# Optimization experiments

Hardware: AMD Instinct MI355X
Metric: run time of the kernel (lower is better)

Reference implementation:

```python
import jax, jax.numpy as jnp
import numpy as np

N_NODES = 50000
N_EDGES = 800000
N_PAIRS = 200000
IN_DIM = 128
HID = 64
OUT_DIM = 1


def _gat_layer(x, W, a_l, a_r, src, dst, n_nodes):
    # Single-head GAT (DGL-style): z = xW; attention logits from learned
    # left/right vectors; softmax over incoming edges of each dst node.
    z = x @ W                                   # [N, H]
    el = z @ a_l                                # [N]
    er = z @ a_r                                # [N]
    e = jax.nn.leaky_relu(el[src] + er[dst], 0.2)   # [E]
    emax = jax.ops.segment_max(e, dst, num_segments=n_nodes)  # [N]
    ex = jnp.exp(e - emax[dst])                 # [E], stable softmax numerator
    denom = jax.ops.segment_sum(ex, dst, num_segments=n_nodes)  # [N]
    msg = ex[:, None] * z[src]                  # [E, H]
    agg = jax.ops.segment_sum(msg, dst, num_segments=n_nodes)   # [N, H]
    return agg / jnp.maximum(denom, 1e-9)[:, None]


def setup_inputs() -> dict:
    key = jax.random.key(0)
    ks = jax.random.split(key, 10)
    feat = jax.random.normal(ks[0], (N_NODES, IN_DIM), dtype=jnp.float32)
    src = jax.random.randint(ks[1], (N_EDGES,), 0, N_NODES, dtype=jnp.int32)
    dst = jax.random.randint(ks[2], (N_EDGES,), 0, N_NODES, dtype=jnp.int32)
    # query pairs: take existing edges so the has_edges_between mask is true
    pair_src = src[:N_PAIRS]
    pair_dst = dst[:N_PAIRS]
    s1 = 1.0 / np.sqrt(IN_DIM)
    s2 = 1.0 / np.sqrt(HID)
    W1 = jax.random.normal(ks[3], (IN_DIM, HID), dtype=jnp.float32) * s1
    al1 = jax.random.normal(ks[4], (HID,), dtype=jnp.float32) * s2
    ar1 = jax.random.normal(ks[5], (HID,), dtype=jnp.float32) * s2
    W2 = jax.random.normal(ks[6], (HID, HID), dtype=jnp.float32) * s2
    al2 = jax.random.normal(ks[7], (HID,), dtype=jnp.float32) * s2
    ar2 = jax.random.normal(ks[8], (HID,), dtype=jnp.float32) * s2
    Wc = jax.random.normal(ks[9], (2 * HID, OUT_DIM), dtype=jnp.float32) * s2
    bc = jnp.zeros((OUT_DIM,), dtype=jnp.float32)
    return {"feat": feat, "W1": W1, "al1": al1, "ar1": ar1,
            "W2": W2, "al2": al2, "ar2": ar2, "Wc": Wc, "bc": bc,
            "src": src, "dst": dst, "pair_src": pair_src, "pair_dst": pair_dst}


def reference(feat, W1, al1, ar1, W2, al2, ar2, Wc, bc, src, dst, pair_src, pair_dst):
    src = src.astype(jnp.int32)
    dst = dst.astype(jnp.int32)
    # two hetero GAT layers (single ntype -> mean aggregate is identity) + ReLU
    h = jax.nn.relu(_gat_layer(feat, W1, al1, ar1, src, dst, N_NODES))
    h = jax.nn.relu(_gat_layer(h, W2, al2, ar2, src, dst, N_NODES))
    # has_edges_between(pair_src, pair_dst): membership test via sorted edge keys
    ekeys = src.astype(jnp.int64) * N_NODES + dst.astype(jnp.int64)
    skeys = jnp.sort(ekeys)
    pkeys = pair_src.astype(jnp.int64) * N_NODES + pair_dst.astype(jnp.int64)
    idx = jnp.clip(jnp.searchsorted(skeys, pkeys), 0, N_EDGES - 1)
    mask = (skeys[idx] == pkeys)                 # [P] bool
    # gather endpoint embeddings, concat, classify, sigmoid; invalid rows -> 0
    hs = h[pair_src]                             # [P, H]
    hd = h[pair_dst]                             # [P, H]
    h_pair = jnp.concatenate([hs, hd], axis=1)   # [P, 2H]
    out = jax.nn.sigmoid(h_pair @ Wc + bc)       # [P, OUT]
    return out * mask[:, None].astype(out.dtype)
```

## Files before the change

kernel.cpp:

```cpp
#include <hip/hip_runtime.h>
#include <cstdint>

#define N_NODES 50000
#define N_EDGES 800000
#define N_PAIRS 200000
#define IN_DIM 128
#define HID 64
#define N_WAVES_GEMM (N_NODES / 16)
#define NBIN 196
#define NCH 320
#define CHUNK ((N_EDGES + NCH - 1) / NCH)
#define MHIST (NBIN * NCH)
#define SBG ((MHIST + 255) / 256)
#define MB_GEMM ((N_WAVES_GEMM + 3) / 4)
#define NODE_BLOCKS ((N_NODES + 3) / 4)
#define MEMBER_BLOCKS (N_PAIRS / 32)
#define SEG_T 1024

typedef __attribute__((ext_vector_type(8))) short bf16x8;
typedef __attribute__((ext_vector_type(4))) float f32x4;

__device__ __forceinline__ unsigned short bf16_rne(float f) {
    unsigned u = __float_as_uint(f);
    unsigned t = u + 0x7FFFu + ((u >> 16) & 1u);
    return (unsigned short)(t >> 16);
}
__device__ __forceinline__ void bf2f(unsigned u, float& a, float& b) {
    a = __uint_as_float(u << 16);
    b = __uint_as_float(u & 0xFFFF0000u);
}

__global__ __launch_bounds__(256) void hist_prep(
    const int* __restrict__ dst, int* __restrict__ histHi,
    const float* __restrict__ W1, const float* __restrict__ W2,
    unsigned short* __restrict__ w1hi, unsigned short* __restrict__ w1lo,
    unsigned short* __restrict__ w2hi, unsigned short* __restrict__ w2lo)
{
    const int t = threadIdx.x, b = blockIdx.x;
    if (b < NCH) {
        __shared__ int hist[256];
        hist[t] = 0; __syncthreads();
        const int beg = b * CHUNK, end = min(beg + CHUNK, N_EDGES);
        for (int e = beg + t; e < end; e += 256) atomicAdd(&hist[dst[e] >> 8], 1);
        __syncthreads();
        if (t < NBIN) histHi[t * NCH + b] = hist[t];
    } else {
        int tid = (b - NCH) * 256 + t;
        if (tid < 8192) {
            int jj = tid & 7, lane = (tid >> 3) & 63, tt = (tid >> 9) & 3, ks = tid >> 11;
            int k = ks * 32 + (lane >> 4) * 8 + jj;
            int n = tt * 16 + (lane & 15);
            float f = W1[k * HID + n];
            unsigned short hi = bf16_rne(f);
            float fhi = __uint_as_float(((unsigned)hi) << 16);
            w1hi[tid] = hi;
            w1lo[tid] = bf16_rne(f - fhi);
        }
        if (tid < 4096) {
            int jj = tid & 7, lane = (tid >> 3) & 63, tt = (tid >> 9) & 3, ks = tid >> 11;
            int k = ks * 32 + (lane >> 4) * 8 + jj;
            int n = tt * 16 + (lane & 15);
            float f = W2[k * HID + n];
            unsigned short hi = bf16_rne(f);
            float fhi = __uint_as_float(((unsigned)hi) << 16);
            w2hi[tid] = hi;
            w2lo[tid] = bf16_rne(f - fhi);
        }
    }
}

__global__ __launch_bounds__(256) void scan1g(
    int* __restrict__ histHi, int* __restrict__ bsums)
{
    __shared__ int sh[256];
    const int t = threadIdx.x;
    const int i = blockIdx.x * 256 + t;
    int v = (i < MHIST) ? histHi[i] : 0;
    sh[t] = v; __syncthreads();
    #pragma unroll
    for (int off = 1; off < 256; off <<= 1) {
        int x = sh[t];
        int a = (t >= off) ? sh[t - off] : 0;
        __syncthreads();
        sh[t] = x + a;
        __syncthreads();
    }
    if (i < MHIST) histHi[i] = sh[t] - v;
    if (t == 255) bsums[blockIdx.x] = sh[255];
}

__device__ __forceinline__ void scan_bsums(const int* __restrict__ bsums,
                                           int* sh, int* exb, int t)
{
    int v = (t < SBG) ? bsums[t] : 0;
    sh[t] = v; __syncthreads();
    #pragma unroll
    for (int off = 1; off < 256; off <<= 1) {
        int x = sh[t];
        int a = (t >= off) ? sh[t - off] : 0;
        __syncthreads();
        sh[t] = x + a;
        __syncthreads();
    }
    exb[t] = sh[t] - v;
    __syncthreads();
}

__device__ __forceinline__ void gemm1_body(
    int wave, int lane,
    const float* __restrict__ x,
    const unsigned short* __restrict__ whi, const unsigned short* __restrict__ wlo,
    const float* __restrict__ al, const float* __restrict__ ar,
    unsigned short* __restrict__ z, float* __restrict__ el, float* __restrict__ er)
{
    const int i0 = wave * 16;
    const int m = lane & 15, quad = lane >> 4;
    f32x4 acc[4] = {{0.f,0.f,0.f,0.f},{0.f,0.f,0.f,0.f},{0.f,0.f,0.f,0.f},{0.f,0.f,0.f,0.f}};
    const float* xrow = x + (size_t)(i0 + m) * IN_DIM;

    #pragma unroll 1
    for (int ks = 0; ks < 4; ++ks) {
        const float4 xv0 = *(const float4*)&xrow[ks * 32 + quad * 8];
        const float4 xv1 = *(const float4*)&xrow[ks * 32 + quad * 8 + 4];
        float xs[8] = {xv0.x, xv0.y, xv0.z, xv0.w, xv1.x, xv1.y, xv1.z, xv1.w};
        bf16x8 ahi, alo;
        #pragma unroll
        for (int jj = 0; jj < 8; ++jj) {
            unsigned short hb = bf16_rne(xs[jj]);
            float fhi = __uint_as_float(((unsigned)hb) << 16);
            ahi[jj] = (short)hb;
            alo[jj] = (short)bf16_rne(xs[jj] - fhi);
        }
        #pragma unroll
        for (int t = 0; t < 4; ++t) {
            const bf16x8 bhi = *(const bf16x8*)&whi[(((ks * 4 + t) * 64) + lane) * 8];
            const bf16x8 blo = *(const bf16x8*)&wlo[(((ks * 4 + t) * 64) + lane) * 8];
            acc[t] = __builtin_amdgcn_mfma_f32_16x16x32_bf16(ahi, bhi, acc[t], 0, 0, 0);
            acc[t] = __builtin_amdgcn_mfma_f32_16x16x32_bf16(ahi, blo, acc[t], 0, 0, 0);
            acc[t] = __builtin_amdgcn_mfma_f32_16x16x32_bf16(alo, bhi, acc[t], 0, 0, 0);
        }
    }
    #pragma unroll
    for (int r = 0; r < 4; ++r) {
        const int row = quad * 4 + r;
        float se = 0.f, sr = 0.f;
        #pragma unroll
        for (int t = 0; t < 4; ++t) {
            float v = acc[t][r];
            z[(size_t)(i0 + row) * HID + t * 16 + m] = bf16_rne(v);
            se = fmaf(v, al[t * 16 + m], se);
            sr = fmaf(v, ar[t * 16 + m], sr);
        }
        #pragma unroll
        for (int off = 1; off < 16; off <<= 1) {
            se += __shfl_xor(se, off, 64);
            sr += __shfl_xor(sr, off, 64);
        }
        if (m == 0) { el[i0 + row] = se; er[i0 + row] = sr; }
    }
}

__global__ __launch_bounds__(256) void scatter_gemm1(
    const int* __restrict__ src, const int* __restrict__ dst,
    const int* __restrict__ histEx, const int* __restrict__ bsums,
    unsigned* __restrict__ pairs,
    const float* __restrict__ x,
    const unsigned short* __restrict__ whi, const unsigned short* __restrict__ wlo,
    const float* __restrict__ al, const float* __restrict__ ar,
    unsigned short* __restrict__ z, float* __restrict__ el, float* __restrict__ er)
{
    const int b = blockIdx.x;
    if (b < NCH) {
        __shared__ int sh[256], exb[256], base[256];
        const int t = threadIdx.y * 64 + threadIdx.x;
        scan_bsums(bsums, sh, exb, t);
        if (t < NBIN) {
            int idx = t * NCH + b;
            base[t] = histEx[idx] + exb[idx >> 8];
        }
        __syncthreads();
        const int beg = b * CHUNK, end = min(beg + CHUNK, N_EDGES);
        for (int e = beg + t; e < end; e += 256) {
            int s = src[e], d = dst[e];
            int pos = atomicAdd(&base[d >> 8], 1);
            pairs[pos] = ((unsigned)s << 16) | (unsigned)d;
        }
    } else {
        const int wave = (b - NCH) * 4 + threadIdx.y;
        if (wave < N_WAVES_GEMM)
            gemm1_body(wave, threadIdx.x, x, whi, wlo, al, ar, z, el, er);
    }
}

__global__ __launch_bounds__(SEG_T) void seg_sort(
    const unsigned* __restrict__ pairs, const int* __restrict__ histEx,
    const int* __restrict__ bsums,
    int* __restrict__ row_start, unsigned short* __restrict__ csr_src)
{
    __shared__ int sh[256], exb[256], hist[256], sc[256], offs[256];
    const int t = threadIdx.x, b = blockIdx.x;

    {
        int v = 0;
        if (t < 256) { v = (t < SBG) ? bsums[t] : 0; sh[t] = v; }
        __syncthreads();
        #pragma unroll
        for (int off = 1; off < 256; off <<= 1) {
            int x = 0, a = 0;
            if (t < 256) { x = sh[t]; a = (t >= off) ? sh[t - off] : 0; }
            __syncthreads();
            if (t < 256) sh[t] = x + a;
            __syncthreads();
        }
        if (t < 256) exb[t] = sh[t] - v;
        __syncthreads();
    }

    const int i0 = b * NCH;
    const int segStart = histEx[i0] + exb[i0 >> 8];
    int segEnd = N_EDGES;
    if (b < NBIN - 1) {
        const int i1 = (b + 1) * NCH;
        segEnd = histEx[i1] + exb[i1 >> 8];
    }

    if (t < 256) hist[t] = 0;
    __syncthreads();
    for (int i = segStart + t; i < segEnd; i += SEG_T)
        atomicAdd(&hist[pairs[i] & 255], 1);
    __syncthreads();

    int v = 0;
    if (t < 256) { v = hist[t]; sc[t] = v; }
    __syncthreads();
    #pragma unroll
    for (int off = 1; off < 256; off <<= 1) {
        int x = 0, a = 0;
        if (t < 256) { x = sc[t]; a = (t >= off) ? sc[t - off] : 0; }
        __syncthreads();
        if (t < 256) sc[t] = x + a;
        __syncthreads();
    }
    if (t < 256) {
        const int excl = sc[t] - v;
        offs[t] = segStart + excl;
        const int node = b * 256 + t;
        if (node <= N_NODES) row_start[node] = segStart + excl;
    }
    __syncthreads();
    for (int i = segStart + t; i < segEnd; i += SEG_T) {
        unsigned p = pairs[i];
        int pos = atomicAdd(&offs[p & 255], 1);
        csr_src[pos] = (unsigned short)(p >> 16);
    }
}

template <bool LAST>
__device__ __forceinline__ void agg_body(
    int i, int lane,
    const int* __restrict__ row_start, const unsigned short* __restrict__ csr_src,
    const float* __restrict__ el, const float* __restrict__ er,
    const unsigned short* __restrict__ z, unsigned short* __restrict__ hdst,
    const float* __restrict__ Wc, float* __restrict__ as, float* __restrict__ ad)
{
    const int rb = row_start[i], re = row_start[i + 1];
    const float er_i = er[i];
    const int es = lane >> 3;
    const int fl = lane & 7;

    float acc[8] = {0.f,0.f,0.f,0.f,0.f,0.f,0.f,0.f};
    float den = 0.f;

    int eA = rb + es;        bool vA = eA < re;
    int eB = eA + 8;         bool vB = eB < re;
    int sA = vA ? (int)csr_src[eA] : 0;
    int sB = vB ? (int)csr_src[eB] : 0;
    float elA = el[sA];
    uint4 zA = ((const uint4*)(z + (size_t)sA * HID))[fl];

    for (int e0 = rb; e0 < re; e0 += 8) {
        const int eC = e0 + 16 + es;
        const bool vC = eC < re;
        const int sC = vC ? (int)csr_src[eC] : 0;
        const float elB = el[sB];
        const uint4 zB = ((const uint4*)(z + (size_t)sB * HID))[fl];

        float x = elA + er_i;
        float lr = x > 0.f ? x : 0.2f * x;
        float ex = vA ? __expf(lr) : 0.f;
        float z0, z1, z2, z3, z4, z5, z6, z7;
        bf2f(zA.x, z0, z1); bf2f(zA.y, z2, z3);
        bf2f(zA.z, z4, z5); bf2f(zA.w, z6, z7);
        acc[0] = fmaf(ex, z0, acc[0]); acc[1] = fmaf(ex, z1, acc[1]);
        acc[2] = fmaf(ex, z2, acc[2]); acc[3] = fmaf(ex, z3, acc[3]);
        acc[4] = fmaf(ex, z4, acc[4]); acc[5] = fmaf(ex, z5, acc[5]);
        acc[6] = fmaf(ex, z6, acc[6]); acc[7] = fmaf(ex, z7, acc[7]);
        den += ex;

        sA = sB; vA = vB; elA = elB; zA = zB;
        sB = sC; vB = vC;
    }
    #pragma unroll
    for (int off = 8; off < 64; off <<= 1) {
        #pragma unroll
        for (int q = 0; q < 8; ++q) acc[q] += __shfl_xor(acc[q], off, 64);
        den += __shfl_xor(den, off, 64);
    }
    if (es == 0) {
        float inv = 1.f / fmaxf(den, 1e-9f);
        float hv[8];
        #pragma unroll
        for (int q = 0; q < 8; ++q) hv[q] = fmaxf(acc[q] * inv, 0.f);
        if (LAST) {
            float ps = 0.f, pd = 0.f;
            #pragma unroll
            for (int q = 0; q < 8; ++q) {
                ps = fmaf(hv[q], Wc[fl * 8 + q], ps);
                pd = fmaf(hv[q], Wc[HID + fl * 8 + q], pd);
            }
            #pragma unroll
            for (int off = 1; off < 8; off <<= 1) {
                ps += __shfl_xor(ps, off, 64);
                pd += __shfl_xor(pd, off, 64);
            }
            if (fl == 0) { as[i] = ps; ad[i] = pd; }
        } else {
            unsigned short o[8];
            #pragma unroll
            for (int q = 0; q < 8; ++q) o[q] = bf16_rne(hv[q]);
            uint4 pk;
            pk.x = (unsigned)o[0] | ((unsigned)o[1] << 16);
            pk.y = (unsigned)o[2] | ((unsigned)o[3] << 16);
            pk.z = (unsigned)o[4] | ((unsigned)o[5] << 16);
            pk.w = (unsigned)o[6] | ((unsigned)o[7] << 16);
            ((uint4*)hdst)[fl] = pk;
        }
    }
}

__global__ __launch_bounds__(256) void agg1_gemm2_member(
    const int* __restrict__ row_start, const unsigned short* __restrict__ csr_src,
    const float* __restrict__ el1, const float* __restrict__ er1,
    const unsigned short* __restrict__ z1,
    const unsigned short* __restrict__ whi, const unsigned short* __restrict__ wlo,
    const float* __restrict__ al, const float* __restrict__ ar,
    unsigned short* __restrict__ z2, float* __restrict__ el2, float* __restrict__ er2,
    const int* __restrict__ ps, const int* __restrict__ pd, int* __restrict__ found)
{
    const int b = blockIdx.x, lane = threadIdx.x, ty = threadIdx.y;
    if (b < N_WAVES_GEMM) {
        __shared__ __align__(16) unsigned short ht[16][72];
        const int i0 = b * 16;
        #pragma unroll 1
        for (int c = 0; c < 4; ++c) {
            const int r = ty * 4 + c;
            agg_body<false>(i0 + r, lane, row_start, csr_src, el1, er1, z1,
                            &ht[r][0], nullptr, nullptr, nullptr);
        }
        __syncthreads();
        if (ty == 0) {
            const int m = lane & 15, quad = lane >> 4;
            f32x4 acc[4] = {{0.f,0.f,0.f,0.f},{0.f,0.f,0.f,0.f},
                            {0.f,0.f,0.f,0.f},{0.f,0.f,0.f,0.f}};
            const unsigned short* xrow = &ht[m][0];
            #pragma unroll 1
            for (int ks = 0; ks < 2; ++ks) {
                const bf16x8 aa = *(const bf16x8*)&xrow[ks * 32 + quad * 8];
                #pragma unroll
                for (int tt = 0; tt < 4; ++tt) {
                    const bf16x8 bhi = *(const bf16x8*)&whi[(((ks * 4 + tt) * 64) + lane) * 8];
                    const bf16x8 blo = *(const bf16x8*)&wlo[(((ks * 4 + tt) * 64) + lane) * 8];
                    acc[tt] = __builtin_amdgcn_mfma_f32_16x16x32_bf16(aa, bhi, acc[tt], 0, 0, 0);
                    acc[tt] = __builtin_amdgcn_mfma_f32_16x16x32_bf16(aa, blo, acc[tt], 0, 0, 0);
                }
            }
            #pragma unroll
            for (int r = 0; r < 4; ++r) {
                const int row = quad * 4 + r;
                float se = 0.f, sr = 0.f;
                #pragma unroll
                for (int tt = 0; tt < 4; ++tt) {
                    float v = acc[tt][r];
                    z2[(size_t)(i0 + row) * HID + tt * 16 + m] = bf16_rne(v);
                    se = fmaf(v, al[tt * 16 + m], se);
                    sr = fmaf(v, ar[tt * 16 + m], sr);
                }
                #pragma unroll
                for (int off = 1; off < 16; off <<= 1) {
                    se += __shfl_xor(se, off, 64);
                    sr += __shfl_xor(sr, off, 64);
                }
                if (m == 0) { el2[i0 + row] = se; er2[i0 + row] = sr; }
            }
        }
    } else {
        const int r8 = lane & 7, g = lane >> 3;
        const int p = (b - N_WAVES_GEMM) * 32 + ty * 8 + g;
        const int s = ps[p], d = pd[p];
        const int rb = row_start[d], re = row_start[d + 1];
        int f = 0;
        for (int e = rb + r8; e < re; e += 8) f |= ((int)csr_src[e] == s) ? 1 : 0;
        #pragma unroll
        for (int off = 1; off < 8; off <<= 1) f |= __shfl_xor(f, off, 64);
        if (r8 == 0) found[p] = f;
    }
}

__global__ __launch_bounds__(256) void agg2(
    const int* __restrict__ row_start, const unsigned short* __restrict__ csr_src,
    const float* __restrict__ el, const float* __restrict__ er,
    const unsigned short* __restrict__ z, const float* __restrict__ Wc,
    float* __restrict__ as, float* __restrict__ ad)
{
    const int i = blockIdx.x * 4 + threadIdx.y;
    if (i < N_NODES)
        agg_body<true>(i, threadIdx.x, row_start, csr_src, el, er, z,
                       nullptr, Wc, as, ad);
}

__global__ __launch_bounds__(256) void pair_tiny(
    const int* __restrict__ ps, const int* __restrict__ pd,
    const float* __restrict__ as, const float* __restrict__ ad,
    const float* __restrict__ bc, const int* __restrict__ found,
    float* __restrict__ out)
{
    const int p = blockIdx.x * 256 + threadIdx.x;
    if (p >= N_PAIRS) return;
    float v = as[ps[p]] + ad[pd[p]] + bc[0];
    float sg = 1.f / (1.f + __expf(-v));
    out[p] = found[p] ? sg : 0.f;
}

extern "C" void kernel_launch(void* const* d_in, const int* in_sizes, int n_in,
                              void* d_out, int out_size, void* d_ws, size_t ws_size,
                              hipStream_t stream)
{
    const float* feat = (const float*)d_in[0];
    const float* W1   = (const float*)d_in[1];
    const float* al1  = (const float*)d_in[2];
    const float* ar1  = (const float*)d_in[3];
    const float* W2   = (const float*)d_in[4];
    const float* al2  = (const float*)d_in[5];
    const float* ar2  = (const float*)d_in[6];
    const float* Wc   = (const float*)d_in[7];
    const float* bc   = (const float*)d_in[8];
    const int* src    = (const int*)d_in[9];
    const int* dst    = (const int*)d_in[10];
    const int* psrc   = (const int*)d_in[11];
    const int* pdst   = (const int*)d_in[12];
    float* out = (float*)d_out;

    char* ws = (char*)d_ws;
    unsigned short* z  = (unsigned short*)ws;  ws += (size_t)N_NODES * HID * 2;
    unsigned short* z2 = (unsigned short*)ws;  ws += (size_t)N_NODES * HID * 2;
    float* el = (float*)ws;               ws += (size_t)N_NODES * 4;
    float* er = (float*)ws;               ws += (size_t)N_NODES * 4;
    float* as = (float*)ws;               ws += (size_t)N_NODES * 4;
    float* ad = (float*)ws;               ws += (size_t)N_NODES * 4;
    float* el2 = (float*)ws;              ws += (size_t)N_NODES * 4;
    float* er2 = (float*)ws;              ws += (size_t)N_NODES * 4;
    int* row_start = (int*)ws;            ws += (size_t)(N_NODES + 1) * 4;
    int* histHi = (int*)ws;               ws += (size_t)MHIST * 4;
    int* bsumsA = (int*)ws;               ws += (size_t)(SBG + 1) * 4;
    int* found = (int*)ws;                ws += (size_t)N_PAIRS * 4;
    ws = (char*)(((uintptr_t)ws + 255) & ~(uintptr_t)255);
    unsigned* pairs = (unsigned*)ws;      ws += (size_t)N_EDGES * 4;
    unsigned short* csr_src = (unsigned short*)ws;  ws += (size_t)N_EDGES * 2;
    ws = (char*)(((uintptr_t)ws + 255) & ~(uintptr_t)255);
    unsigned short* w1hi = (unsigned short*)ws;  ws += 8192 * 2;
    unsigned short* w1lo = (unsigned short*)ws;  ws += 8192 * 2;
    unsigned short* w2hi = (unsigned short*)ws;  ws += 4096 * 2;
    unsigned short* w2lo = (unsigned short*)ws;  ws += 4096 * 2;

    dim3 b64x4(64, 4);

    hist_prep<<<NCH + 32, 256, 0, stream>>>(dst, histHi, W1, W2, w1hi, w1lo, w2hi, w2lo);
    scan1g<<<SBG, 256, 0, stream>>>(histHi, bsumsA);
    scatter_gemm1<<<NCH + MB_GEMM, b64x4, 0, stream>>>(src, dst, histHi, bsumsA, pairs,
        feat, w1hi, w1lo, al1, ar1, z, el, er);
    seg_sort<<<NBIN, SEG_T, 0, stream>>>(pairs, histHi, bsumsA, row_start, csr_src);
    agg1_gemm2_member<<<N_WAVES_GEMM + MEMBER_BLOCKS, b64x4, 0, stream>>>(
        row_start, csr_src, el, er, z, w2hi, w2lo, al2, ar2,
        z2, el2, er2, psrc, pdst, found);
    agg2<<<NODE_BLOCKS, b64x4, 0, stream>>>(row_start, csr_src, el2, er2, z2, Wc, as, ad);
    pair_tiny<<<(N_PAIRS + 255) / 256, 256, 0, stream>>>(psrc, pdst, as, ad, bc, found, out);
}
```

Baseline: 182.1 us.

## Replace histogram+scan bucketing with fixed-capacity per-chunk bucket slots

```diff
diff --git a/kernel.cpp b/kernel.cpp
--- a/kernel.cpp
+++ b/kernel.cpp
@@ -10,8 +10,7 @@
 #define NBIN 196
 #define NCH 320
 #define CHUNK ((N_EDGES + NCH - 1) / NCH)
-#define MHIST (NBIN * NCH)
-#define SBG ((MHIST + 255) / 256)
+#define CAP 64
 #define MB_GEMM ((N_WAVES_GEMM + 3) / 4)
 #define NODE_BLOCKS ((N_NODES + 3) / 4)
 #define MEMBER_BLOCKS (N_PAIRS / 32)
@@ -30,80 +29,32 @@
     b = __uint_as_float(u & 0xFFFF0000u);
 }
 
-__global__ __launch_bounds__(256) void hist_prep(
-    const int* __restrict__ dst, int* __restrict__ histHi,
+__global__ __launch_bounds__(256) void prep(
     const float* __restrict__ W1, const float* __restrict__ W2,
     unsigned short* __restrict__ w1hi, unsigned short* __restrict__ w1lo,
     unsigned short* __restrict__ w2hi, unsigned short* __restrict__ w2lo)
 {
-    const int t = threadIdx.x, b = blockIdx.x;
-    if (b < NCH) {
-        __shared__ int hist[256];
-        hist[t] = 0; __syncthreads();
-        const int beg = b * CHUNK, end = min(beg + CHUNK, N_EDGES);
-        for (int e = beg + t; e < end; e += 256) atomicAdd(&hist[dst[e] >> 8], 1);
-        __syncthreads();
-        if (t < NBIN) histHi[t * NCH + b] = hist[t];
-    } else {
-        int tid = (b - NCH) * 256 + t;
-        if (tid < 8192) {
-            int jj = tid & 7, lane = (tid >> 3) & 63, tt = (tid >> 9) & 3, ks = tid >> 11;
-            int k = ks * 32 + (lane >> 4) * 8 + jj;
-            int n = tt * 16 + (lane & 15);
-            float f = W1[k * HID + n];
-            unsigned short hi = bf16_rne(f);
-            float fhi = __uint_as_float(((unsigned)hi) << 16);
-            w1hi[tid] = hi;
-            w1lo[tid] = bf16_rne(f - fhi);
-        }
-        if (tid < 4096) {
-            int jj = tid & 7, lane = (tid >> 3) & 63, tt = (tid >> 9) & 3, ks = tid >> 11;
-            int k = ks * 32 + (lane >> 4) * 8 + jj;
-            int n = tt * 16 + (lane & 15);
-            float f = W2[k * HID + n];
-            unsigned short hi = bf16_rne(f);
-            float fhi = __uint_as_float(((unsigned)hi) << 16);
-            w2hi[tid] = hi;
-            w2lo[tid] = bf16_rne(f - fhi);
-        }
-    }
-}
-
-__global__ __launch_bounds__(256) void scan1g(
-    int* __restrict__ histHi, int* __restrict__ bsums)
-{
-    __shared__ int sh[256];
-    const int t = threadIdx.x;
-    const int i = blockIdx.x * 256 + t;
-    int v = (i < MHIST) ? histHi[i] : 0;
-    sh[t] = v; __syncthreads();
-    #pragma unroll
-    for (int off = 1; off < 256; off <<= 1) {
-        int x = sh[t];
-        int a = (t >= off) ? sh[t - off] : 0;
-        __syncthreads();
-        sh[t] = x + a;
-        __syncthreads();
-    }
-    if (i < MHIST) histHi[i] = sh[t] - v;
-    if (t == 255) bsums[blockIdx.x] = sh[255];
-}
-
-__device__ __forceinline__ void scan_bsums(const int* __restrict__ bsums,
-                                           int* sh, int* exb, int t)
-{
-    int v = (t < SBG) ? bsums[t] : 0;
-    sh[t] = v; __syncthreads();
-    #pragma unroll
-    for (int off = 1; off < 256; off <<= 1) {
-        int x = sh[t];
-        int a = (t >= off) ? sh[t - off] : 0;
-        __syncthreads();
-        sh[t] = x + a;
-        __syncthreads();
-    }
-    exb[t] = sh[t] - v;
-    __syncthreads();
+    int tid = blockIdx.x * 256 + threadIdx.x;
+    if (tid < 8192) {
+        int jj = tid & 7, lane = (tid >> 3) & 63, tt = (tid >> 9) & 3, ks = tid >> 11;
+        int k = ks * 32 + (lane >> 4) * 8 + jj;
+        int n = tt * 16 + (lane & 15);
+        float f = W1[k * HID + n];
+        unsigned short hi = bf16_rne(f);
+        float fhi = __uint_as_float(((unsigned)hi) << 16);
+        w1hi[tid] = hi;
+        w1lo[tid] = bf16_rne(f - fhi);
+    }
+    if (tid < 4096) {
+        int jj = tid & 7, lane = (tid >> 3) & 63, tt = (tid >> 9) & 3, ks = tid >> 11;
+        int k = ks * 32 + (lane >> 4) * 8 + jj;
+        int n = tt * 16 + (lane & 15);
+        float f = W2[k * HID + n];
+        unsigned short hi = bf16_rne(f);
+        float fhi = __uint_as_float(((unsigned)hi) << 16);
+        w2hi[tid] = hi;
+        w2lo[tid] = bf16_rne(f - fhi);
+    }
 }
 
 __device__ __forceinline__ void gemm1_body(
@@ -162,8 +113,7 @@
 
 __global__ __launch_bounds__(256) void scatter_gemm1(
     const int* __restrict__ src, const int* __restrict__ dst,
-    const int* __restrict__ histEx, const int* __restrict__ bsums,
-    unsigned* __restrict__ pairs,
+    unsigned* __restrict__ pairs, int* __restrict__ cnt,
     const float* __restrict__ x,
     const unsigned short* __restrict__ whi, const unsigned short* __restrict__ wlo,
     const float* __restrict__ al, const float* __restrict__ ar,
@@ -171,20 +121,18 @@
 {
     const int b = blockIdx.x;
     if (b < NCH) {
-        __shared__ int sh[256], exb[256], base[256];
+        __shared__ int lcnt[256];
         const int t = threadIdx.y * 64 + threadIdx.x;
-        scan_bsums(bsums, sh, exb, t);
-        if (t < NBIN) {
-            int idx = t * NCH + b;
-            base[t] = histEx[idx] + exb[idx >> 8];
-        }
-        __syncthreads();
+        lcnt[t] = 0; __syncthreads();
         const int beg = b * CHUNK, end = min(beg + CHUNK, N_EDGES);
         for (int e = beg + t; e < end; e += 256) {
             int s = src[e], d = dst[e];
-            int pos = atomicAdd(&base[d >> 8], 1);
-            pairs[pos] = ((unsigned)s << 16) | (unsigned)d;
-        }
+            int bin = d >> 8;
+            int slot = atomicAdd(&lcnt[bin], 1);
+            pairs[((size_t)bin * NCH + b) * CAP + slot] = ((unsigned)s << 16) | (unsigned)d;
+        }
+        __syncthreads();
+        cnt[t * NCH + b] = lcnt[t];
     } else {
         const int wave = (b - NCH) * 4 + threadIdx.y;
         if (wave < N_WAVES_GEMM)
@@ -193,41 +141,61 @@
 }
 
 __global__ __launch_bounds__(SEG_T) void seg_sort(
-    const unsigned* __restrict__ pairs, const int* __restrict__ histEx,
-    const int* __restrict__ bsums,
+    const unsigned* __restrict__ pairs, const int* __restrict__ cnt,
     int* __restrict__ row_start, unsigned short* __restrict__ csr_src)
 {
-    __shared__ int sh[256], exb[256], hist[256], sc[256], offs[256];
+    __shared__ int cnts[NCH], cs[512], cpre[NCH + 1];
+    __shared__ int hist[256], sc[256], offs[256];
+    __shared__ int redu[16];
+    __shared__ int segStartSh;
     const int t = threadIdx.x, b = blockIdx.x;
+
+    if (t < NCH) cnts[t] = cnt[b * NCH + t];
+
+    {
+        int s = 0;
+        const int n = b * NCH;
+        for (int i = t; i < n; i += SEG_T) s += cnt[i];
+        #pragma unroll
+        for (int off = 32; off >= 1; off >>= 1) s += __shfl_down(s, off, 64);
+        if ((t & 63) == 0) redu[t >> 6] = s;
+        __syncthreads();
+        if (t == 0) {
+            int tot = 0;
+            #pragma unroll
+            for (int w = 0; w < 16; ++w) tot += redu[w];
+            segStartSh = tot;
+        }
+        __syncthreads();
+    }
+    const int segStart = segStartSh;
 
     {
         int v = 0;
-        if (t < 256) { v = (t < SBG) ? bsums[t] : 0; sh[t] = v; }
-        __syncthreads();
-        #pragma unroll
-        for (int off = 1; off < 256; off <<= 1) {
+        if (t < 512) { v = (t < NCH) ? cnts[t] : 0; cs[t] = v; }
+        __syncthreads();
+        #pragma unroll
+        for (int off = 1; off < 512; off <<= 1) {
             int x = 0, a = 0;
-            if (t < 256) { x = sh[t]; a = (t >= off) ? sh[t - off] : 0; }
+            if (t < 512) { x = cs[t]; a = (t >= off) ? cs[t - off] : 0; }
             __syncthreads();
-            if (t < 256) sh[t] = x + a;
+            if (t < 512) cs[t] = x + a;
             __syncthreads();
         }
-        if (t < 256) exb[t] = sh[t] - v;
-        __syncthreads();
-    }
-
-    const int i0 = b * NCH;
-    const int segStart = histEx[i0] + exb[i0 >> 8];
-    int segEnd = N_EDGES;
-    if (b < NBIN - 1) {
-        const int i1 = (b + 1) * NCH;
-        segEnd = histEx[i1] + exb[i1 >> 8];
-    }
+        if (t < NCH) cpre[t] = cs[t] - v;
+        if (t == 0) cpre[NCH] = cs[511];
+        __syncthreads();
+    }
+    const int segLen = cpre[NCH];
 
     if (t < 256) hist[t] = 0;
     __syncthreads();
-    for (int i = segStart + t; i < segEnd; i += SEG_T)
-        atomicAdd(&hist[pairs[i] & 255], 1);
+    for (int p = t; p < segLen; p += SEG_T) {
+        int lo = 0, hi = NCH - 1;
+        while (lo < hi) { int mid = (lo + hi + 1) >> 1; if (cpre[mid] <= p) lo = mid; else hi = mid - 1; }
+        unsigned pr = pairs[((size_t)b * NCH + lo) * CAP + (p - cpre[lo])];
+        atomicAdd(&hist[pr & 255], 1);
+    }
     __syncthreads();
 
     int v = 0;
@@ -248,10 +216,13 @@
         if (node <= N_NODES) row_start[node] = segStart + excl;
     }
     __syncthreads();
-    for (int i = segStart + t; i < segEnd; i += SEG_T) {
-        unsigned p = pairs[i];
-        int pos = atomicAdd(&offs[p & 255], 1);
-        csr_src[pos] = (unsigned short)(p >> 16);
+
+    for (int p = t; p < segLen; p += SEG_T) {
+        int lo = 0, hi = NCH - 1;
+        while (lo < hi) { int mid = (lo + hi + 1) >> 1; if (cpre[mid] <= p) lo = mid; else hi = mid - 1; }
+        unsigned pr = pairs[((size_t)b * NCH + lo) * CAP + (p - cpre[lo])];
+        int pos = atomicAdd(&offs[pr & 255], 1);
+        csr_src[pos] = (unsigned short)(pr >> 16);
     }
 }
 
@@ -460,11 +431,10 @@
     float* el2 = (float*)ws;              ws += (size_t)N_NODES * 4;
     float* er2 = (float*)ws;              ws += (size_t)N_NODES * 4;
     int* row_start = (int*)ws;            ws += (size_t)(N_NODES + 1) * 4;
-    int* histHi = (int*)ws;               ws += (size_t)MHIST * 4;
-    int* bsumsA = (int*)ws;               ws += (size_t)(SBG + 1) * 4;
+    int* cnt = (int*)ws;                  ws += (size_t)256 * NCH * 4;
     int* found = (int*)ws;                ws += (size_t)N_PAIRS * 4;
     ws = (char*)(((uintptr_t)ws + 255) & ~(uintptr_t)255);
-    unsigned* pairs = (unsigned*)ws;      ws += (size_t)N_EDGES * 4;
+    unsigned* pairs = (unsigned*)ws;      ws += (size_t)NBIN * NCH * CAP * 4;
     unsigned short* csr_src = (unsigned short*)ws;  ws += (size_t)N_EDGES * 2;
     ws = (char*)(((uintptr_t)ws + 255) & ~(uintptr_t)255);
     unsigned short* w1hi = (unsigned short*)ws;  ws += 8192 * 2;
@@ -474,11 +444,10 @@
 
     dim3 b64x4(64, 4);
 
-    hist_prep<<<NCH + 32, 256, 0, stream>>>(dst, histHi, W1, W2, w1hi, w1lo, w2hi, w2lo);
-    scan1g<<<SBG, 256, 0, stream>>>(histHi, bsumsA);
-    scatter_gemm1<<<NCH + MB_GEMM, b64x4, 0, stream>>>(src, dst, histHi, bsumsA, pairs,
+    prep<<<32, 256, 0, stream>>>(W1, W2, w1hi, w1lo, w2hi, w2lo);
+    scatter_gemm1<<<NCH + MB_GEMM, b64x4, 0, stream>>>(src, dst, pairs, cnt,
         feat, w1hi, w1lo, al1, ar1, z, el, er);
-    seg_sort<<<NBIN, SEG_T, 0, stream>>>(pairs, histHi, bsumsA, row_start, csr_src);
+    seg_sort<<<NBIN, SEG_T, 0, stream>>>(pairs, cnt, row_start, csr_src);
     agg1_gemm2_member<<<N_WAVES_GEMM + MEMBER_BLOCKS, b64x4, 0, stream>>>(
         row_start, csr_src, el, er, z, w2hi, w2lo, al2, ar2,
         z2, el2, er2, psrc, pdst, found);
```

After: 190.3 us. 4.5% more time.
